# Optimization experiments

Hardware: AMD Instinct MI355X
Metric: run time of the kernel (lower is better)

## Reference

```python
import jax, jax.numpy as jnp
import numpy as np

N_NODES = 100000
N_EDGES = 1600000
DIMS = [512, 200, 175, 125, 75, 50]


def setup_inputs() -> dict:
    key = jax.random.key(0)
    ks = jax.random.split(key, 12)
    inp = {
        "x": jax.random.normal(ks[0], (N_NODES, DIMS[0]), dtype=jnp.float32),
        "edge_index": jax.random.randint(ks[1], (2, N_EDGES), 0, N_NODES, dtype=jnp.int32),
    }
    for i in range(5):
        fan_in, fan_out = DIMS[i], DIMS[i + 1]
        scale = 1.0 / np.sqrt(fan_in)
        inp[f"W{i+1}"] = jax.random.uniform(ks[2 + 2 * i], (fan_in, fan_out), minval=-scale, maxval=scale, dtype=jnp.float32)
        inp[f"b{i+1}"] = jnp.zeros((fan_out,), dtype=jnp.float32)
    return inp


def _gcn_norm(edge_index, n_nodes):
    # add self loops, then symmetric normalization D^-1/2 (A+I) D^-1/2
    loop = jnp.arange(n_nodes, dtype=edge_index.dtype)
    src = jnp.concatenate([edge_index[0], loop])
    dst = jnp.concatenate([edge_index[1], loop])
    deg = jax.ops.segment_sum(jnp.ones_like(dst, dtype=jnp.float32), dst, num_segments=n_nodes)
    dinv = jnp.where(deg > 0, jax.lax.rsqrt(deg), 0.0)
    norm = dinv[src] * dinv[dst]  # [E+N]
    return src, dst, norm


def _gcn_layer(x, W, b, src, dst, norm, n_nodes):
    h = x @ W                                   # [N, out] dense GEMM
    msg = h[src] * norm[:, None]                # gather + scale  [E+N, out]
    agg = jax.ops.segment_sum(msg, dst, num_segments=n_nodes)  # scatter-add
    return agg + b


def reference(x, edge_index, W1, b1, W2, b2, W3, b3, W4, b4, W5, b5):
    n = x.shape[0]
    src, dst, norm = _gcn_norm(edge_index, n)
    h = jax.nn.relu(_gcn_layer(x, W1, b1, src, dst, norm, n))
    h = jax.nn.relu(_gcn_layer(h, W2, b2, src, dst, norm, n))
    h = jax.nn.relu(_gcn_layer(h, W3, b3, src, dst, norm, n))
    h = jax.nn.relu(_gcn_layer(h, W4, b4, src, dst, norm, n))
    return _gcn_layer(h, W5, b5, src, dst, norm, n)
```

## Files before the change

### kernel.cpp

```cpp
#include <hip/hip_runtime.h>
#include <hip/hip_bf16.h>


typedef float f32x4 __attribute__((ext_vector_type(4)));
typedef short bf16x8 __attribute__((ext_vector_type(8)));

static const int GDIMS[6] = {512, 200, 175, 125, 75, 50};
static const int GPAD[6]  = {512, 224, 192, 128, 96, 64};


__global__ void zero_kernel(int* __restrict__ p, int n) {
    int i = blockIdx.x * blockDim.x + threadIdx.x;
    for (; i < n; i += gridDim.x * blockDim.x) p[i] = 0;
}

__global__ void hist_kernel(const int* __restrict__ dst, int E, int* __restrict__ deg) {
    int i = blockIdx.x * blockDim.x + threadIdx.x;
    for (; i < E; i += gridDim.x * blockDim.x) atomicAdd(&deg[dst[i]], 1);
}

__global__ __launch_bounds__(1024) void scan_kernel(const int* __restrict__ deg,
                                                    int* __restrict__ rowptr, int N) {
    __shared__ int sums[1024];
    int t = threadIdx.x;
    int chunk = (N + 1023) >> 10;
    int lo = t * chunk;
    int hi = lo + chunk; if (hi > N) hi = N;
    if (lo > N) lo = N;
    int s = 0;
    for (int i = lo; i < hi; ++i) s += deg[i];
    sums[t] = s;
    __syncthreads();
    for (int off = 1; off < 1024; off <<= 1) {
        int v = (t >= off) ? sums[t - off] : 0;
        __syncthreads();
        sums[t] += v;
        __syncthreads();
    }
    int run = (t > 0) ? sums[t - 1] : 0;
    for (int i = lo; i < hi; ++i) { rowptr[i] = run; run += deg[i]; }
    if (t == 1023) rowptr[N] = run;
}

__global__ void dinv_kernel(const int* __restrict__ deg, float* __restrict__ dinv, int N) {
    int i = blockIdx.x * blockDim.x + threadIdx.x;
    for (; i < N; i += gridDim.x * blockDim.x)
        dinv[i] = rsqrtf((float)(deg[i] + 1));
}

__global__ void copy_kernel(const int* __restrict__ a, int* __restrict__ b, int n) {
    int i = blockIdx.x * blockDim.x + threadIdx.x;
    for (; i < n; i += gridDim.x * blockDim.x) b[i] = a[i];
}

__global__ void scatter_kernel(const int* __restrict__ src, const int* __restrict__ dst,
                               int E, int* __restrict__ cursor, int* __restrict__ csrc) {
    int i = blockIdx.x * blockDim.x + threadIdx.x;
    for (; i < E; i += gridDim.x * blockDim.x) {
        int d = dst[i];
        int pos = atomicAdd(&cursor[d], 1);
        csrc[pos] = src[i];
    }
}


__global__ void wsplit_kernel(const float* __restrict__ W, int K, int Nout,
                              int Kp, ushort* __restrict__ Whi, ushort* __restrict__ Wlo) {
    int k = blockIdx.x * blockDim.x + threadIdx.x;
    int n = blockIdx.y;
    if (k >= Kp) return;
    float v = (k < K && n < Nout) ? W[(size_t)k * Nout + n] : 0.f;
    __bf16 h = (__bf16)v;
    float hf = (float)h;
    __bf16 l = (__bf16)(v - hf);
    Whi[(size_t)n * Kp + k] = __builtin_bit_cast(ushort, h);
    Wlo[(size_t)n * Kp + k] = __builtin_bit_cast(ushort, l);
}


__device__ inline f32x4 mfma16(bf16x8 a, bf16x8 b, f32x4 c) {
    return __builtin_amdgcn_mfma_f32_16x16x32_bf16(a, b, c, 0, 0, 0);
}

__device__ inline void split_frag(f32x4 a0, f32x4 a1, bf16x8& hi, bf16x8& lo) {
    float af[8];
    af[0] = a0[0]; af[1] = a0[1]; af[2] = a0[2]; af[3] = a0[3];
    af[4] = a1[0]; af[5] = a1[1]; af[6] = a1[2]; af[7] = a1[3];
#pragma unroll
    for (int e = 0; e < 8; ++e) {
        __bf16 h = (__bf16)af[e];
        float hf = (float)h;
        __bf16 l = (__bf16)(af[e] - hf);
        hi[e] = __builtin_bit_cast(short, h);
        lo[e] = __builtin_bit_cast(short, l);
    }
}

__global__ __launch_bounds__(256) void gemm_mfma(
    const float* __restrict__ A, int lda, int Mrows,
    const ushort* __restrict__ Bhi, const ushort* __restrict__ Blo, int Kp,
    float* __restrict__ C, int ldc, int Pout)
{
    int lane = threadIdx.x & 63;
    int wave = threadIdx.x >> 6;
    int m0 = blockIdx.x * 256 + wave * 64;
    int n0 = blockIdx.y * 64;
    int koff = (lane >> 4) * 8;

    const float* aptr[4];
#pragma unroll
    for (int fm = 0; fm < 4; ++fm) {
        int row = m0 + fm * 16 + (lane & 15);
        if (row > Mrows - 1) row = Mrows - 1;
        aptr[fm] = A + (size_t)row * lda + koff;
    }
    const ushort* bhp[4];
#pragma unroll
    for (int fn = 0; fn < 4; ++fn) {
        int n = n0 + fn * 16 + (lane & 15);
        bhp[fn] = Bhi + (size_t)n * Kp + koff;
    }
    size_t lo_off = (size_t)(Blo - Bhi);

    f32x4 acc[4][4];
#pragma unroll
    for (int i = 0; i < 4; ++i)
#pragma unroll
        for (int j = 0; j < 4; ++j) acc[i][j] = (f32x4)0.f;

    for (int k0 = 0; k0 < Kp; k0 += 32) {
        bf16x8 vbh[4], vbl[4];
#pragma unroll
        for (int fn = 0; fn < 4; ++fn) {
            vbh[fn] = *(const bf16x8*)(bhp[fn] + k0);
            vbl[fn] = *(const bf16x8*)(bhp[fn] + lo_off + k0);
        }
        bf16x8 vah[4], val[4];
#pragma unroll
        for (int fm = 0; fm < 4; ++fm) {
            f32x4 a0 = *(const f32x4*)(aptr[fm] + k0);
            f32x4 a1 = *(const f32x4*)(aptr[fm] + k0 + 4);
            split_frag(a0, a1, vah[fm], val[fm]);
        }
#pragma unroll
        for (int fm = 0; fm < 4; ++fm)
#pragma unroll
            for (int fn = 0; fn < 4; ++fn) {
                acc[fm][fn] = mfma16(vah[fm], vbh[fn], acc[fm][fn]);
                acc[fm][fn] = mfma16(vah[fm], vbl[fn], acc[fm][fn]);
                acc[fm][fn] = mfma16(val[fm], vbh[fn], acc[fm][fn]);
            }
    }

#pragma unroll
    for (int fm = 0; fm < 4; ++fm) {
#pragma unroll
        for (int fn = 0; fn < 4; ++fn) {
            int col = n0 + fn * 16 + (lane & 15);
            if (col < Pout) {
#pragma unroll
                for (int r = 0; r < 4; ++r) {
                    int row = m0 + fm * 16 + (lane >> 4) * 4 + r;
                    C[(size_t)row * ldc + col] = acc[fm][fn][r];
                }
            }
        }
    }
}


__global__ __launch_bounds__(256) void agg_kernel(
    const float* __restrict__ h, int ldh,
    const int* __restrict__ rowptr, const int* __restrict__ csrc,
    const float* __restrict__ dinv, const float* __restrict__ bias,
    int D, int N, int Mp, float* __restrict__ out, int ldo,
    int L, int relu, int final_layer)
{
    int tid = threadIdx.x;
    int node = blockIdx.x * (256 / L) + tid / L;
    if (node >= Mp) return;
    int f4 = tid & (L - 1);
    int ld4 = ldh >> 2;
    bool act = f4 < ld4;

    const f32x4* h4 = (const f32x4*)h;
    f32x4 acc = (f32x4)0.f;
    float di = 0.f;
    if (node < N) {
        di = dinv[node];
        if (act) acc = di * h4[(size_t)node * ld4 + f4];
        int beg = rowptr[node];
        int end = rowptr[node + 1];
        for (int j = beg; j < end; ++j) {
            int s = csrc[j];
            float ds = dinv[s];
            if (act) acc += ds * h4[(size_t)s * ld4 + f4];
        }
    }

    if (final_layer) {
        if (node >= N) return;
#pragma unroll
        for (int e = 0; e < 4; ++e) {
            int f = f4 * 4 + e;
            if (f < D) out[(size_t)node * ldo + f] = fmaf(di, acc[e], bias[f]);
        }
    } else {
        if (!act) return;
        f32x4 v;
#pragma unroll
        for (int e = 0; e < 4; ++e) {
            int f = f4 * 4 + e;
            float val = 0.f;
            if (node < N && f < D) {
                val = fmaf(di, acc[e], bias[f]);
                if (relu) val = fmaxf(val, 0.f);
            }
            v[e] = val;
        }
        *(f32x4*)(out + (size_t)node * ldo + f4 * 4) = v;
    }
}


extern "C" void kernel_launch(void* const* d_in, const int* in_sizes, int n_in,
                              void* d_out, int out_size, void* d_ws, size_t ws_size,
                              hipStream_t stream) {
    const float* x = (const float*)d_in[0];
    const int* ei = (const int*)d_in[1];
    int E = in_sizes[1] / 2;
    int N = in_sizes[0] / GDIMS[0];
    int Mp = ((N + 255) / 256) * 256;
    const int* src = ei;
    const int* dst = ei + E;

    const float* W[5];
    const float* bia[5];
    for (int i = 0; i < 5; ++i) {
        W[i] = (const float*)d_in[2 + 2 * i];
        bia[i] = (const float*)d_in[3 + 2 * i];
    }

    char* ws = (char*)d_ws;
    size_t off = 0;
    auto alloc = [&](size_t bytes) -> void* {
        void* p = ws + off;
        off += (bytes + 255) & ~(size_t)255;
        return p;
    };
    int* deg = (int*)alloc((size_t)N * 4);
    int* rowptr = (int*)alloc((size_t)(N + 1) * 4);
    int* cursor = (int*)alloc((size_t)N * 4);
    float* dinv = (float*)alloc((size_t)N * 4);
    int* csrc = (int*)alloc((size_t)E * 4);
    float* buf0 = (float*)alloc((size_t)Mp * 224 * 4);
    float* buf1 = (float*)alloc((size_t)Mp * 224 * 4);
    ushort* Whi[5];
    ushort* Wlo[5];
    int NB[5];
    for (int l = 0; l < 5; ++l) {
        int Kp = GPAD[l];
        NB[l] = ((GPAD[l + 1] + 63) / 64) * 64;
        Whi[l] = (ushort*)alloc((size_t)NB[l] * Kp * 2);
        Wlo[l] = (ushort*)alloc((size_t)NB[l] * Kp * 2);
    }
    (void)ws_size;

    zero_kernel<<<1024, 256, 0, stream>>>(deg, N);
    hist_kernel<<<2048, 256, 0, stream>>>(dst, E, deg);
    scan_kernel<<<1, 1024, 0, stream>>>(deg, rowptr, N);
    dinv_kernel<<<512, 256, 0, stream>>>(deg, dinv, N);
    copy_kernel<<<512, 256, 0, stream>>>(rowptr, cursor, N);
    scatter_kernel<<<2048, 256, 0, stream>>>(src, dst, E, cursor, csrc);

    for (int l = 0; l < 5; ++l) {
        int Kp = GPAD[l];
        dim3 g((Kp + 255) / 256, NB[l]);
        wsplit_kernel<<<g, 256, 0, stream>>>(W[l], GDIMS[l], GDIMS[l + 1], Kp,
                                             Whi[l], Wlo[l]);
    }

    for (int l = 0; l < 5; ++l) {
        int Kp = GPAD[l];
        int Pout = GPAD[l + 1];
        int D = GDIMS[l + 1];
        const float* Ain = (l == 0) ? x : buf1;
        int lda = Kp;
        int Mrows = (l == 0) ? N : Mp;

        dim3 gg(Mp / 256, (Pout + 63) / 64);
        gemm_mfma<<<gg, 256, 0, stream>>>(Ain, lda, Mrows, Whi[l], Wlo[l], Kp,
                                          buf0, Pout, Pout);

        int ld4 = Pout / 4;
        int L = (ld4 > 32) ? 64 : (ld4 > 16) ? 32 : 16;
        int nodes_per_block = 256 / L;
        int blocks = (Mp + nodes_per_block - 1) / nodes_per_block;
        if (l == 4) {
            agg_kernel<<<blocks, 256, 0, stream>>>(buf0, Pout, rowptr, csrc, dinv,
                                                   bia[l], D, N, Mp, (float*)d_out, D,
                                                   L, 0, 1);
        } else {
            agg_kernel<<<blocks, 256, 0, stream>>>(buf0, Pout, rowptr, csrc, dinv,
                                                   bia[l], D, N, Mp, buf1, Pout,
                                                   L, 1, 0);
        }
    }
    (void)out_size; (void)n_in;
}
```

Baseline: 1.514 ms.

## Stage A tiles in LDS across wide-N GEMM blocks, fold source dinv into GEMM epilogue

The GEMM now converts and splits each A tile into bf16 hi/lo once per block and stages it in shared memory. Waves in the block share that tile and cover the full output width, so A is read once instead of once per 64-column block. The source-side dinv scale moves into the GEMM epilogue, so the aggregation kernel only sums gathered rows, using four independent accumulators and templated lane widths, and skips padded feature columns and padded nodes. This adds block syncs per k-step and LDS traffic, and the per-layer wave shapes are hand-picked.

```diff
diff --git a/kernel.cpp b/kernel.cpp
--- a/kernel.cpp
+++ b/kernel.cpp
@@ -71,9 +71,10 @@
     if (k >= Kp) return;
     float v = (k < K && n < Nout) ? W[(size_t)k * Nout + n] : 0.f;
     __bf16 h = (__bf16)v;
-    float hf = (float)h;
+    ushort hb = __builtin_bit_cast(ushort, h);
+    float hf = __builtin_bit_cast(float, (unsigned)hb << 16);
     __bf16 l = (__bf16)(v - hf);
-    Whi[(size_t)n * Kp + k] = __builtin_bit_cast(ushort, h);
+    Whi[(size_t)n * Kp + k] = hb;
     Wlo[(size_t)n * Kp + k] = __builtin_bit_cast(ushort, l);
 }
 
@@ -82,45 +83,48 @@
     return __builtin_amdgcn_mfma_f32_16x16x32_bf16(a, b, c, 0, 0, 0);
 }
 
-__device__ inline void split_frag(f32x4 a0, f32x4 a1, bf16x8& hi, bf16x8& lo) {
-    float af[8];
-    af[0] = a0[0]; af[1] = a0[1]; af[2] = a0[2]; af[3] = a0[3];
-    af[4] = a1[0]; af[5] = a1[1]; af[6] = a1[2]; af[7] = a1[3];
+__device__ inline void split8(f32x4 a0, f32x4 a1, bf16x8& hi, bf16x8& lo) {
+    float af[8] = {a0[0], a0[1], a0[2], a0[3], a1[0], a1[1], a1[2], a1[3]};
 #pragma unroll
     for (int e = 0; e < 8; ++e) {
         __bf16 h = (__bf16)af[e];
-        float hf = (float)h;
+        ushort hb = __builtin_bit_cast(ushort, h);
+        float hf = __builtin_bit_cast(float, (unsigned)hb << 16);
         __bf16 l = (__bf16)(af[e] - hf);
-        hi[e] = __builtin_bit_cast(short, h);
+        hi[e] = (short)hb;
         lo[e] = __builtin_bit_cast(short, l);
     }
 }
 
-__global__ __launch_bounds__(256) void gemm_mfma(
-    const float* __restrict__ A, int lda, int Mrows,
+template<int WM, int WN>
+__global__ __launch_bounds__(WM * WN * 64) void gemm_t(
+    const float* __restrict__ A, int lda, int Arows,
     const ushort* __restrict__ Bhi, const ushort* __restrict__ Blo, int Kp,
-    float* __restrict__ C, int ldc, int Pout)
+    const float* __restrict__ dinv, int N,
+    float* __restrict__ C, int ldc)
 {
-    int lane = threadIdx.x & 63;
-    int wave = threadIdx.x >> 6;
-    int m0 = blockIdx.x * 256 + wave * 64;
-    int n0 = blockIdx.y * 64;
-    int koff = (lane >> 4) * 8;
-
-    const float* aptr[4];
-#pragma unroll
-    for (int fm = 0; fm < 4; ++fm) {
-        int row = m0 + fm * 16 + (lane & 15);
-        if (row > Mrows - 1) row = Mrows - 1;
-        aptr[fm] = A + (size_t)row * lda + koff;
-    }
-    const ushort* bhp[4];
+    constexpr int BM = WM * 64;
+    constexpr int T = WM * WN * 64;
+    constexpr int SROW = BM + 2;
+    __shared__ ushort Ah[4 * SROW * 8];
+    __shared__ ushort Al[4 * SROW * 8];
+
+    const int tid = threadIdx.x;
+    const int lane = tid & 63;
+    const int wave = tid >> 6;
+    const int wm = (WM == 1) ? 0 : (wave % WM);
+    const int wn = (WM == 1) ? wave : (wave / WM);
+    const int m0 = blockIdx.x * BM;
+    const int kg = lane >> 4;
+    const int l16 = lane & 15;
+
+    const ushort* bp[4];
 #pragma unroll
     for (int fn = 0; fn < 4; ++fn) {
-        int n = n0 + fn * 16 + (lane & 15);
-        bhp[fn] = Bhi + (size_t)n * Kp + koff;
-    }
-    size_t lo_off = (size_t)(Blo - Bhi);
+        int n = wn * 64 + fn * 16 + l16;
+        bp[fn] = Bhi + (size_t)n * Kp + kg * 8;
+    }
+    const size_t lo_off = (size_t)(Blo - Bhi);
 
     f32x4 acc[4][4];
 #pragma unroll
@@ -129,93 +133,109 @@
         for (int j = 0; j < 4; ++j) acc[i][j] = (f32x4)0.f;
 
     for (int k0 = 0; k0 < Kp; k0 += 32) {
-        bf16x8 vbh[4], vbl[4];
+        for (int j = tid; j < BM * 4; j += T) {
+            int row = j >> 2, jk = j & 3;
+            int gr = m0 + row; if (gr > Arows - 1) gr = Arows - 1;
+            const float* ap = A + (size_t)gr * lda + k0 + jk * 8;
+            f32x4 a0 = *(const f32x4*)ap;
+            f32x4 a1 = *(const f32x4*)(ap + 4);
+            bf16x8 hi, lo;
+            split8(a0, a1, hi, lo);
+            int idx = (jk * SROW + row) * 8;
+            *(bf16x8*)&Ah[idx] = hi;
+            *(bf16x8*)&Al[idx] = lo;
+        }
+        __syncthreads();
+
+        bf16x8 bh[4], bl[4], ah[4], al[4];
 #pragma unroll
         for (int fn = 0; fn < 4; ++fn) {
-            vbh[fn] = *(const bf16x8*)(bhp[fn] + k0);
-            vbl[fn] = *(const bf16x8*)(bhp[fn] + lo_off + k0);
-        }
-        bf16x8 vah[4], val[4];
+            bh[fn] = *(const bf16x8*)(bp[fn] + k0);
+            bl[fn] = *(const bf16x8*)(bp[fn] + lo_off + k0);
+        }
 #pragma unroll
         for (int fm = 0; fm < 4; ++fm) {
-            f32x4 a0 = *(const f32x4*)(aptr[fm] + k0);
-            f32x4 a1 = *(const f32x4*)(aptr[fm] + k0 + 4);
-            split_frag(a0, a1, vah[fm], val[fm]);
+            int idx = (kg * SROW + wm * 64 + fm * 16 + l16) * 8;
+            ah[fm] = *(const bf16x8*)&Ah[idx];
+            al[fm] = *(const bf16x8*)&Al[idx];
         }
 #pragma unroll
         for (int fm = 0; fm < 4; ++fm)
 #pragma unroll
             for (int fn = 0; fn < 4; ++fn) {
-                acc[fm][fn] = mfma16(vah[fm], vbh[fn], acc[fm][fn]);
-                acc[fm][fn] = mfma16(vah[fm], vbl[fn], acc[fm][fn]);
-                acc[fm][fn] = mfma16(val[fm], vbh[fn], acc[fm][fn]);
+                acc[fm][fn] = mfma16(ah[fm], bh[fn], acc[fm][fn]);
+                acc[fm][fn] = mfma16(ah[fm], bl[fn], acc[fm][fn]);
+                acc[fm][fn] = mfma16(al[fm], bh[fn], acc[fm][fn]);
             }
-    }
-
-#pragma unroll
-    for (int fm = 0; fm < 4; ++fm) {
+        __syncthreads();
+    }
+
+    float dv[4][4];
+#pragma unroll
+    for (int fm = 0; fm < 4; ++fm)
+#pragma unroll
+        for (int r = 0; r < 4; ++r) {
+            int row = m0 + wm * 64 + fm * 16 + kg * 4 + r;
+            dv[fm][r] = (row < N) ? dinv[row] : 0.f;
+        }
+#pragma unroll
+    for (int fm = 0; fm < 4; ++fm)
 #pragma unroll
         for (int fn = 0; fn < 4; ++fn) {
-            int col = n0 + fn * 16 + (lane & 15);
-            if (col < Pout) {
+            int col = wn * 64 + fn * 16 + l16;
+            if (col < ldc) {
 #pragma unroll
                 for (int r = 0; r < 4; ++r) {
-                    int row = m0 + fm * 16 + (lane >> 4) * 4 + r;
-                    C[(size_t)row * ldc + col] = acc[fm][fn][r];
+                    int row = m0 + wm * 64 + fm * 16 + kg * 4 + r;
+                    C[(size_t)row * ldc + col] = acc[fm][fn][r] * dv[fm][r];
                 }
             }
         }
-    }
-}
-
-
-__global__ __launch_bounds__(256) void agg_kernel(
-    const float* __restrict__ h, int ldh,
+}
+
+
+template<int L>
+__global__ __launch_bounds__(256) void agg_t(
+    const float* __restrict__ g, int ldg, int nd4,
     const int* __restrict__ rowptr, const int* __restrict__ csrc,
     const float* __restrict__ dinv, const float* __restrict__ bias,
-    int D, int N, int Mp, float* __restrict__ out, int ldo,
-    int L, int relu, int final_layer)
+    int D, int N, float* __restrict__ out, int ldo, int relu, int fin)
 {
-    int tid = threadIdx.x;
-    int node = blockIdx.x * (256 / L) + tid / L;
-    if (node >= Mp) return;
-    int f4 = tid & (L - 1);
-    int ld4 = ldh >> 2;
-    bool act = f4 < ld4;
-
-    const f32x4* h4 = (const f32x4*)h;
-    f32x4 acc = (f32x4)0.f;
-    float di = 0.f;
-    if (node < N) {
-        di = dinv[node];
-        if (act) acc = di * h4[(size_t)node * ld4 + f4];
-        int beg = rowptr[node];
-        int end = rowptr[node + 1];
-        for (int j = beg; j < end; ++j) {
-            int s = csrc[j];
-            float ds = dinv[s];
-            if (act) acc += ds * h4[(size_t)s * ld4 + f4];
-        }
-    }
-
-    if (final_layer) {
-        if (node >= N) return;
+    int node = blockIdx.x * (256 / L) + threadIdx.x / L;
+    if (node >= N) return;
+    int f4 = threadIdx.x & (L - 1);
+    if (f4 >= nd4) return;
+
+    const f32x4* g4 = (const f32x4*)g;
+    int ld4 = ldg >> 2;
+    f32x4 a0 = g4[(size_t)node * ld4 + f4];
+    f32x4 a1 = (f32x4)0.f, a2 = (f32x4)0.f, a3 = (f32x4)0.f;
+    int beg = rowptr[node], end = rowptr[node + 1];
+    int j = beg;
+    for (; j + 3 < end; j += 4) {
+        int s0 = csrc[j], s1 = csrc[j + 1], s2 = csrc[j + 2], s3 = csrc[j + 3];
+        a0 += g4[(size_t)s0 * ld4 + f4];
+        a1 += g4[(size_t)s1 * ld4 + f4];
+        a2 += g4[(size_t)s2 * ld4 + f4];
+        a3 += g4[(size_t)s3 * ld4 + f4];
+    }
+    for (; j < end; ++j) a0 += g4[(size_t)csrc[j] * ld4 + f4];
+
+    f32x4 s = (a0 + a1) + (a2 + a3);
+    float di = dinv[node];
+    if (fin) {
 #pragma unroll
         for (int e = 0; e < 4; ++e) {
             int f = f4 * 4 + e;
-            if (f < D) out[(size_t)node * ldo + f] = fmaf(di, acc[e], bias[f]);
+            if (f < D) out[(size_t)node * ldo + f] = fmaf(di, s[e], bias[f]);
         }
     } else {
-        if (!act) return;
         f32x4 v;
 #pragma unroll
         for (int e = 0; e < 4; ++e) {
             int f = f4 * 4 + e;
-            float val = 0.f;
-            if (node < N && f < D) {
-                val = fmaf(di, acc[e], bias[f]);
-                if (relu) val = fmaxf(val, 0.f);
-            }
+            float val = (f < D) ? fmaf(di, s[e], bias[f]) : 0.f;
+            if (relu) val = fmaxf(val, 0.f);
             v[e] = val;
         }
         *(f32x4*)(out + (size_t)node * ldo + f4 * 4) = v;
@@ -261,6 +281,7 @@
     for (int l = 0; l < 5; ++l) {
         int Kp = GPAD[l];
         NB[l] = ((GPAD[l + 1] + 63) / 64) * 64;
+        if (l == 0) NB[l] = 256;
         Whi[l] = (ushort*)alloc((size_t)NB[l] * Kp * 2);
         Wlo[l] = (ushort*)alloc((size_t)NB[l] * Kp * 2);
     }
@@ -275,9 +296,9 @@
 
     for (int l = 0; l < 5; ++l) {
         int Kp = GPAD[l];
-        dim3 g((Kp + 255) / 256, NB[l]);
-        wsplit_kernel<<<g, 256, 0, stream>>>(W[l], GDIMS[l], GDIMS[l + 1], Kp,
-                                             Whi[l], Wlo[l]);
+        dim3 gw((Kp + 255) / 256, NB[l]);
+        wsplit_kernel<<<gw, 256, 0, stream>>>(W[l], GDIMS[l], GDIMS[l + 1], Kp,
+                                              Whi[l], Wlo[l]);
     }
 
     for (int l = 0; l < 5; ++l) {
@@ -285,25 +306,42 @@
         int Pout = GPAD[l + 1];
         int D = GDIMS[l + 1];
         const float* Ain = (l == 0) ? x : buf1;
-        int lda = Kp;
-        int Mrows = (l == 0) ? N : Mp;
-
-        dim3 gg(Mp / 256, (Pout + 63) / 64);
-        gemm_mfma<<<gg, 256, 0, stream>>>(Ain, lda, Mrows, Whi[l], Wlo[l], Kp,
-                                          buf0, Pout, Pout);
-
-        int ld4 = Pout / 4;
-        int L = (ld4 > 32) ? 64 : (ld4 > 16) ? 32 : 16;
-        int nodes_per_block = 256 / L;
-        int blocks = (Mp + nodes_per_block - 1) / nodes_per_block;
-        if (l == 4) {
-            agg_kernel<<<blocks, 256, 0, stream>>>(buf0, Pout, rowptr, csrc, dinv,
-                                                   bia[l], D, N, Mp, (float*)d_out, D,
-                                                   L, 0, 1);
+        int lda = GPAD[l];
+
+        if (l == 0) {
+            gemm_t<1, 4><<<Mp / 64, 256, 0, stream>>>(Ain, lda, N, Whi[l], Wlo[l], Kp,
+                                                      dinv, N, buf0, Pout);
+        } else if (l == 1) {
+            gemm_t<1, 3><<<Mp / 64, 192, 0, stream>>>(Ain, lda, N, Whi[l], Wlo[l], Kp,
+                                                      dinv, N, buf0, Pout);
+        } else if (l == 2 || l == 3) {
+            gemm_t<2, 2><<<Mp / 128, 256, 0, stream>>>(Ain, lda, N, Whi[l], Wlo[l], Kp,
+                                                       dinv, N, buf0, Pout);
         } else {
-            agg_kernel<<<blocks, 256, 0, stream>>>(buf0, Pout, rowptr, csrc, dinv,
-                                                   bia[l], D, N, Mp, buf1, Pout,
-                                                   L, 1, 0);
+            gemm_t<4, 1><<<Mp / 256, 256, 0, stream>>>(Ain, lda, N, Whi[l], Wlo[l], Kp,
+                                                       dinv, N, buf0, Pout);
+        }
+
+        int nd4 = (D + 3) / 4;
+        float* outp = (l == 4) ? (float*)d_out : buf1;
+        int ldo = (l == 4) ? D : Pout;
+        int relu = (l < 4) ? 1 : 0;
+        int fin = (l == 4) ? 1 : 0;
+        if (l <= 1) {
+            int npb = 256 / 64;
+            agg_t<64><<<(N + npb - 1) / npb, 256, 0, stream>>>(buf0, Pout, nd4, rowptr,
+                                                               csrc, dinv, bia[l], D, N,
+                                                               outp, ldo, relu, fin);
+        } else if (l <= 3) {
+            int npb = 256 / 32;
+            agg_t<32><<<(N + npb - 1) / npb, 256, 0, stream>>>(buf0, Pout, nd4, rowptr,
+                                                               csrc, dinv, bia[l], D, N,
+                                                               outp, ldo, relu, fin);
+        } else {
+            int npb = 256 / 16;
+            agg_t<16><<<(N + npb - 1) / npb, 256, 0, stream>>>(buf0, Pout, nd4, rowptr,
+                                                               csrc, dinv, bia[l], D, N,
+                                                               outp, ldo, relu, fin);
         }
     }
     (void)out_size; (void)n_in;
```

New measurement: 1.294 ms. 1.17x faster.
